# Performance work log

Measured on AMD Instinct MI355X. Metric: run time of the kernel, lower is better.

## Reference

```python
import jax, jax.numpy as jnp
import numpy as np

NH, NP, NL, ED = 8, 8, 1, 256  # num_heads, num_sam_pts, num_levels, embed_dim
EPS = 1e-5


def setup_inputs() -> dict:
    key = jax.random.key(0)
    ks = jax.random.split(key, 6)
    bs, h, w = 8, 64, 64
    d = ED // NH
    return {
        "query": jax.random.normal(ks[0], (bs, 1, ED), jnp.float32),
        "single_feat": jax.random.normal(ks[1], (bs, h * w, NH, d), jnp.float32),
        "ref_2d": jax.random.uniform(ks[2], (bs, h * w, NL, 2), jnp.float32),
        "W_off": jax.random.normal(ks[3], (ED, NH * NL * NP * 2), jnp.float32) * 0.02,
        "b_off": jnp.zeros((NH * NL * NP * 2,), jnp.float32),
        "W_attn": jax.random.normal(ks[4], (ED, NH * NL * NP), jnp.float32) * 0.02,
        "b_attn": jnp.zeros((NH * NL * NP,), jnp.float32),
        "ln_g": jnp.ones((ED,), jnp.float32),
        "ln_b": jnp.zeros((ED,), jnp.float32),
        "h": h,
        "w": w,
    }


def reference(query, single_feat, ref_2d, W_off, b_off, W_attn, b_attn, ln_g, ln_b, h, w):
    bs, nq, _, d = single_feat.shape
    # query: [bs,1,ED] repeated over all h*w query positions
    q = jnp.broadcast_to(query, (bs, h * w, ED))

    # sampling offsets (relu'd, normalized by (w,h)) added to reference points
    off = jax.nn.relu(q @ W_off + b_off).reshape(bs, nq, NH, NL, NP, 2)
    offset_normalizer = jnp.array([w, h], dtype=q.dtype)  # (w, h) order as in torch
    loc = ref_2d[:, :, None, :, None, :] + off / offset_normalizer  # [bs,nq,NH,NL,NP,2]

    # attention weights: relu then softmax over points (last axis)
    aw = jax.nn.relu(q @ W_attn + b_attn).reshape(bs, nq, NH, NL, NP)
    aw = jax.nn.softmax(aw, axis=-1)

    # single-level bilinear grid_sample (align_corners=False, zero padding)
    g = 2.0 * loc[:, :, :, 0] - 1.0  # level 0 -> [bs,nq,NH,NP,2]
    x = (g[..., 0] + 1.0) * (w / 2.0) - 0.5  # pixel coords
    y = (g[..., 1] + 1.0) * (h / 2.0) - 0.5
    x0 = jnp.floor(x)
    y0 = jnp.floor(y)
    x0i = x0.astype(jnp.int32)
    y0i = y0.astype(jnp.int32)

    v = single_feat.transpose(0, 2, 1, 3)  # [bs,NH,H*W,d]

    def gather(xi, yi):
        valid = (xi >= 0) & (xi < w) & (yi >= 0) & (yi < h)  # [bs,nq,NH,NP]
        idx = jnp.clip(yi, 0, h - 1) * w + jnp.clip(xi, 0, w - 1)
        idx = idx.transpose(0, 2, 1, 3).reshape(bs, NH, nq * NP, 1)
        s = jnp.take_along_axis(v, idx, axis=2).reshape(bs, NH, nq, NP, d)
        return s * valid.transpose(0, 2, 1, 3)[..., None].astype(s.dtype)

    wx = (x - x0).transpose(0, 2, 1, 3)[..., None]  # [bs,NH,nq,NP,1]
    wy = (y - y0).transpose(0, 2, 1, 3)[..., None]
    s00 = gather(x0i, y0i)
    s01 = gather(x0i + 1, y0i)
    s10 = gather(x0i, y0i + 1)
    s11 = gather(x0i + 1, y0i + 1)
    top = s00 * (1.0 - wx) + s01 * wx
    bot = s10 * (1.0 - wx) + s11 * wx
    sampled = top * (1.0 - wy) + bot * wy  # [bs,NH,nq,NP,d]

    # weighted sum over points, merge heads
    out = jnp.einsum('bhqpd,bqhp->bqhd', sampled, aw[:, :, :, 0]).reshape(bs, nq, NH * d)

    # norm(dropout(output) + query) -- dropout is identity in eval mode
    res = out + q
    mu = res.mean(-1, keepdims=True)
    var = res.var(-1, keepdims=True)
    return (res - mu) / jnp.sqrt(var + EPS) * ln_g + ln_b
```

## Files before the change

kernel.cpp:

```cpp
#include <hip/hip_runtime.h>

#define ED 256
#define NHEAD 8
#define NPTS 8
#define DHEAD 32

__global__ __launch_bounds__(256) void precompute_kernel(
    const float* __restrict__ query,
    const float* __restrict__ W_off, const float* __restrict__ b_off,
    const float* __restrict__ W_attn, const float* __restrict__ b_attn,
    float* __restrict__ ws)
{
    const int b = blockIdx.x;
    const int t = threadIdx.x;
    __shared__ float sq[ED];
    __shared__ float sattn[NHEAD * NPTS];

    sq[t] = query[b * ED + t];
    __syncthreads();

    if (t < 128) {
        float a0 = 0.f, a1 = 0.f, a2 = 0.f, a3 = 0.f;
        #pragma unroll 4
        for (int k = 0; k < ED; k += 4) {
            a0 = fmaf(sq[k + 0], W_off[(k + 0) * 128 + t], a0);
            a1 = fmaf(sq[k + 1], W_off[(k + 1) * 128 + t], a1);
            a2 = fmaf(sq[k + 2], W_off[(k + 2) * 128 + t], a2);
            a3 = fmaf(sq[k + 3], W_off[(k + 3) * 128 + t], a3);
        }
        ws[b * 192 + t] = fmaxf(b_off[t] + ((a0 + a1) + (a2 + a3)), 0.0f);
    } else if (t < 192) {
        const int j = t - 128;
        float a0 = 0.f, a1 = 0.f, a2 = 0.f, a3 = 0.f;
        #pragma unroll 4
        for (int k = 0; k < ED; k += 4) {
            a0 = fmaf(sq[k + 0], W_attn[(k + 0) * 64 + j], a0);
            a1 = fmaf(sq[k + 1], W_attn[(k + 1) * 64 + j], a1);
            a2 = fmaf(sq[k + 2], W_attn[(k + 2) * 64 + j], a2);
            a3 = fmaf(sq[k + 3], W_attn[(k + 3) * 64 + j], a3);
        }
        sattn[j] = fmaxf(b_attn[j] + ((a0 + a1) + (a2 + a3)), 0.0f);
    }
    __syncthreads();

    if (t >= 128 && t < 192) {
        const int j = t - 128;
        const int hh = j >> 3;
        float m = -1e30f;
        #pragma unroll
        for (int p = 0; p < NPTS; ++p) m = fmaxf(m, sattn[hh * NPTS + p]);
        float s = 0.0f;
        #pragma unroll
        for (int p = 0; p < NPTS; ++p) s += expf(sattn[hh * NPTS + p] - m);
        ws[b * 192 + 128 + j] = expf(sattn[j] - m) / s;
    }
}

__global__ __launch_bounds__(256) void deform_attn_kernel(
    const float* __restrict__ feat,
    const float* __restrict__ ref2d,
    const float* __restrict__ query,
    const float* __restrict__ ln_g, const float* __restrict__ ln_b,
    const float* __restrict__ ws,
    const int* __restrict__ Hp, const int* __restrict__ Wp,
    float* __restrict__ out,
    int nq, int bs)
{
    const int blk = blockIdx.x;
    const int b = blk % bs;
    const int qgroup = blk / bs;
    const int t = threadIdx.x;

    __shared__ float s_off[128];
    __shared__ float s_aw[64];
    __shared__ float s_ref[8];
    __shared__ __align__(16) float s_c[4 * 64 * 8];

    if (t < 128)      s_off[t] = ws[b * 192 + t];
    else if (t < 192) s_aw[t - 128] = ws[b * 192 + t];
    else if (t < 200) {
        const int i = t - 192;
        s_ref[i] = ref2d[(b * nq + qgroup * 4 + (i >> 1)) * 2 + (i & 1)];
    }
    const int H = Hp[0];
    const int W = Wp[0];
    __syncthreads();

    {
        const int qL = t >> 6;
        const int hp = t & 63;
        const int p  = hp & 7;
        const int h  = hp >> 3;

        const float x = s_ref[qL * 2 + 0] * (float)W - 0.5f + s_off[hp * 2 + 0];
        const float y = s_ref[qL * 2 + 1] * (float)H - 0.5f + s_off[hp * 2 + 1];
        const float aw = s_aw[hp];

        const float xf = floorf(x);
        const float yf = floorf(y);
        const int ix = (int)xf;
        const int iy = (int)yf;
        const float wx = x - xf;
        const float wy = y - yf;

        const bool vx0 = (ix >= 0) && (ix < W);
        const bool vx1 = (ix + 1 >= 0) && (ix + 1 < W);
        const bool vy0 = (iy >= 0) && (iy < H);
        const bool vy1 = (iy + 1 >= 0) && (iy + 1 < H);
        const int cx0 = min(max(ix, 0), W - 1);
        const int cx1 = min(max(ix + 1, 0), W - 1);
        const int cy0 = min(max(iy, 0), H - 1);
        const int cy1 = min(max(iy + 1, 0), H - 1);

        const int r0 = cy0 * W;
        const int r1 = cy1 * W;
        int4 idx;
        idx.x = r0 + cx0;
        idx.y = r0 + cx1;
        idx.z = r1 + cx0;
        idx.w = r1 + cx1;

        const float awx = aw * wx, awix = aw - awx;
        float4 wt;
        wt.x = (vx0 && vy0) ? awix * (1.0f - wy) : 0.0f;
        wt.y = (vx1 && vy0) ? awx  * (1.0f - wy) : 0.0f;
        wt.z = (vx0 && vy1) ? awix * wy          : 0.0f;
        wt.w = (vx1 && vy1) ? awx  * wy          : 0.0f;

        const int e = ((qL * 8 + p) * 8 + h) * 8;
        *(int4*)  (&s_c[e])     = idx;
        *(float4*)(&s_c[e + 4]) = wt;
    }
    __syncthreads();

    const int qL   = t >> 6;
    const int lane = t & 63;
    const int h    = lane >> 3;
    const int c4   = lane & 7;
    const int q    = qgroup * 4 + qL;

    const float* fb = feat + (size_t)b * nq * ED + h * DHEAD + c4 * 4;

    float ax = 0.f, ay = 0.f, az = 0.f, aww = 0.f;
    #pragma unroll
    for (int p = 0; p < NPTS; ++p) {
        const int e = ((qL * 8 + p) * 8 + h) * 8;
        const int4   idx = *(const int4*)  (&s_c[e]);
        const float4 wt  = *(const float4*)(&s_c[e + 4]);

        const float4 v0 = *(const float4*)(fb + (size_t)idx.x * ED);
        const float4 v1 = *(const float4*)(fb + (size_t)idx.y * ED);
        const float4 v2 = *(const float4*)(fb + (size_t)idx.z * ED);
        const float4 v3 = *(const float4*)(fb + (size_t)idx.w * ED);

        ax = fmaf(wt.x, v0.x, ax); ay = fmaf(wt.x, v0.y, ay);
        az = fmaf(wt.x, v0.z, az); aww = fmaf(wt.x, v0.w, aww);
        ax = fmaf(wt.y, v1.x, ax); ay = fmaf(wt.y, v1.y, ay);
        az = fmaf(wt.y, v1.z, az); aww = fmaf(wt.y, v1.w, aww);
        ax = fmaf(wt.z, v2.x, ax); ay = fmaf(wt.z, v2.y, ay);
        az = fmaf(wt.z, v2.z, az); aww = fmaf(wt.z, v2.w, aww);
        ax = fmaf(wt.w, v3.x, ax); ay = fmaf(wt.w, v3.y, ay);
        az = fmaf(wt.w, v3.z, az); aww = fmaf(wt.w, v3.w, aww);
    }

    const float4 qv = *(const float4*)(query + b * ED + lane * 4);
    const float r0 = ax + qv.x;
    const float r1 = ay + qv.y;
    const float r2 = az + qv.z;
    const float r3 = aww + qv.w;

    float s  = (r0 + r1) + (r2 + r3);
    float ss = fmaf(r0, r0, fmaf(r1, r1, fmaf(r2, r2, r3 * r3)));
    #pragma unroll
    for (int m = 1; m < 64; m <<= 1) {
        s  += __shfl_xor(s, m, 64);
        ss += __shfl_xor(ss, m, 64);
    }
    const float mean = s * (1.0f / ED);
    const float var  = ss * (1.0f / ED) - mean * mean;
    const float inv  = rsqrtf(var + 1e-5f);

    const float4 g = *(const float4*)(ln_g + lane * 4);
    const float4 be = *(const float4*)(ln_b + lane * 4);
    float4 o;
    o.x = (r0 - mean) * inv * g.x + be.x;
    o.y = (r1 - mean) * inv * g.y + be.y;
    o.z = (r2 - mean) * inv * g.z + be.z;
    o.w = (r3 - mean) * inv * g.w + be.w;
    *(float4*)(out + ((size_t)b * nq + q) * ED + lane * 4) = o;
}

extern "C" void kernel_launch(void* const* d_in, const int* in_sizes, int n_in,
                              void* d_out, int out_size, void* d_ws, size_t ws_size,
                              hipStream_t stream)
{
    const float* query  = (const float*)d_in[0];
    const float* feat   = (const float*)d_in[1];
    const float* ref2d  = (const float*)d_in[2];
    const float* W_off  = (const float*)d_in[3];
    const float* b_off  = (const float*)d_in[4];
    const float* W_attn = (const float*)d_in[5];
    const float* b_attn = (const float*)d_in[6];
    const float* ln_g   = (const float*)d_in[7];
    const float* ln_b   = (const float*)d_in[8];
    const int*   Hp     = (const int*)d_in[9];
    const int*   Wp     = (const int*)d_in[10];
    float* out = (float*)d_out;
    float* ws  = (float*)d_ws;

    const int bs = in_sizes[0] / ED;
    const int nq = in_sizes[2] / (bs * 2);

    precompute_kernel<<<bs, 256, 0, stream>>>(query, W_off, b_off, W_attn, b_attn, ws);
    deform_attn_kernel<<<bs * nq / 4, 256, 0, stream>>>(feat, ref2d, query, ln_g, ln_b,
                                                        ws, Hp, Wp, out, nq, bs);
}
```

Before: 145.5 us.

## Process eight queries per block and software-pipeline feature gathers across points

Each block now handles eight query positions instead of four, looping twice over groups of four per thread and hoisting the query, gamma and beta loads out of the loop. Inside the point loop, the gathers for the next sampling point are issued before the FMAs on the current one, so load latency overlaps with arithmetic. The aim is to amortise per-block setup and improve memory-level parallelism. The cost is more registers, a larger shared buffer and half as many blocks, which may reduce occupancy and parallelism.

```diff
diff --git a/kernel.cpp b/kernel.cpp
--- a/kernel.cpp
+++ b/kernel.cpp
@@ -4,6 +4,7 @@
 #define NHEAD 8
 #define NPTS 8
 #define DHEAD 32
+#define QPB 8
 
 __global__ __launch_bounds__(256) void precompute_kernel(
     const float* __restrict__ query,
@@ -68,27 +69,28 @@
 {
     const int blk = blockIdx.x;
     const int b = blk % bs;
-    const int qgroup = blk / bs;
+    const int qbase = (blk / bs) * QPB;
     const int t = threadIdx.x;
 
     __shared__ float s_off[128];
     __shared__ float s_aw[64];
-    __shared__ float s_ref[8];
-    __shared__ __align__(16) float s_c[4 * 64 * 8];
+    __shared__ float s_ref[QPB * 2];
+    __shared__ __align__(16) float s_c[QPB * 64 * 8];
 
     if (t < 128)      s_off[t] = ws[b * 192 + t];
     else if (t < 192) s_aw[t - 128] = ws[b * 192 + t];
-    else if (t < 200) {
+    else if (t < 192 + QPB * 2) {
         const int i = t - 192;
-        s_ref[i] = ref2d[(b * nq + qgroup * 4 + (i >> 1)) * 2 + (i & 1)];
+        s_ref[i] = ref2d[(b * nq + qbase + (i >> 1)) * 2 + (i & 1)];
     }
     const int H = Hp[0];
     const int W = Wp[0];
     __syncthreads();
 
-    {
-        const int qL = t >> 6;
-        const int hp = t & 63;
+    #pragma unroll
+    for (int u = t; u < QPB * 64; u += 256) {
+        const int qL = u >> 6;
+        const int hp = u & 63;
         const int p  = hp & 7;
         const int h  = hp >> 3;
 
@@ -127,7 +129,7 @@
         wt.z = (vx0 && vy1) ? awix * wy          : 0.0f;
         wt.w = (vx1 && vy1) ? awx  * wy          : 0.0f;
 
-        const int e = ((qL * 8 + p) * 8 + h) * 8;
+        const int e = (qL * 64 + p * 8 + h) * 8;
         *(int4*)  (&s_c[e])     = idx;
         *(float4*)(&s_c[e + 4]) = wt;
     }
@@ -137,57 +139,77 @@
     const int lane = t & 63;
     const int h    = lane >> 3;
     const int c4   = lane & 7;
-    const int q    = qgroup * 4 + qL;
 
     const float* fb = feat + (size_t)b * nq * ED + h * DHEAD + c4 * 4;
-
-    float ax = 0.f, ay = 0.f, az = 0.f, aww = 0.f;
+    const float4 qv = *(const float4*)(query + b * ED + lane * 4);
+    const float4 g  = *(const float4*)(ln_g + lane * 4);
+    const float4 be = *(const float4*)(ln_b + lane * 4);
+
     #pragma unroll
-    for (int p = 0; p < NPTS; ++p) {
-        const int e = ((qL * 8 + p) * 8 + h) * 8;
-        const int4   idx = *(const int4*)  (&s_c[e]);
-        const float4 wt  = *(const float4*)(&s_c[e + 4]);
-
-        const float4 v0 = *(const float4*)(fb + (size_t)idx.x * ED);
-        const float4 v1 = *(const float4*)(fb + (size_t)idx.y * ED);
-        const float4 v2 = *(const float4*)(fb + (size_t)idx.z * ED);
-        const float4 v3 = *(const float4*)(fb + (size_t)idx.w * ED);
-
-        ax = fmaf(wt.x, v0.x, ax); ay = fmaf(wt.x, v0.y, ay);
-        az = fmaf(wt.x, v0.z, az); aww = fmaf(wt.x, v0.w, aww);
-        ax = fmaf(wt.y, v1.x, ax); ay = fmaf(wt.y, v1.y, ay);
-        az = fmaf(wt.y, v1.z, az); aww = fmaf(wt.y, v1.w, aww);
-        ax = fmaf(wt.z, v2.x, ax); ay = fmaf(wt.z, v2.y, ay);
-        az = fmaf(wt.z, v2.z, az); aww = fmaf(wt.z, v2.w, aww);
-        ax = fmaf(wt.w, v3.x, ax); ay = fmaf(wt.w, v3.y, ay);
-        az = fmaf(wt.w, v3.z, az); aww = fmaf(wt.w, v3.w, aww);
-    }
-
-    const float4 qv = *(const float4*)(query + b * ED + lane * 4);
-    const float r0 = ax + qv.x;
-    const float r1 = ay + qv.y;
-    const float r2 = az + qv.z;
-    const float r3 = aww + qv.w;
-
-    float s  = (r0 + r1) + (r2 + r3);
-    float ss = fmaf(r0, r0, fmaf(r1, r1, fmaf(r2, r2, r3 * r3)));
-    #pragma unroll
-    for (int m = 1; m < 64; m <<= 1) {
-        s  += __shfl_xor(s, m, 64);
-        ss += __shfl_xor(ss, m, 64);
-    }
-    const float mean = s * (1.0f / ED);
-    const float var  = ss * (1.0f / ED) - mean * mean;
-    const float inv  = rsqrtf(var + 1e-5f);
-
-    const float4 g = *(const float4*)(ln_g + lane * 4);
-    const float4 be = *(const float4*)(ln_b + lane * 4);
-    float4 o;
-    o.x = (r0 - mean) * inv * g.x + be.x;
-    o.y = (r1 - mean) * inv * g.y + be.y;
-    o.z = (r2 - mean) * inv * g.z + be.z;
-    o.w = (r3 - mean) * inv * g.w + be.w;
-    *(float4*)(out + ((size_t)b * nq + q) * ED + lane * 4) = o;
+    for (int gq = 0; gq < QPB / 4; ++gq) {
+        const int qloc = gq * 4 + qL;
+        const int q = qbase + qloc;
+        const int cb = qloc * 512;
+
+        float ax = 0.f, ay = 0.f, az = 0.f, aw4 = 0.f;
+
+        int4   idxA = *(const int4*)  (&s_c[cb + h * 8]);
+        float4 wtA  = *(const float4*)(&s_c[cb + h * 8 + 4]);
+        float4 v0 = *(const float4*)(fb + (size_t)idxA.x * ED);
+        float4 v1 = *(const float4*)(fb + (size_t)idxA.y * ED);
+        float4 v2 = *(const float4*)(fb + (size_t)idxA.z * ED);
+        float4 v3 = *(const float4*)(fb + (size_t)idxA.w * ED);
+
+        #pragma unroll
+        for (int p = 0; p < NPTS; ++p) {
+            int4 idxB; float4 wtB;
+            float4 u0, u1, u2, u3;
+            if (p < NPTS - 1) {
+                const int e = cb + (p + 1) * 64 + h * 8;
+                idxB = *(const int4*)  (&s_c[e]);
+                wtB  = *(const float4*)(&s_c[e + 4]);
+                u0 = *(const float4*)(fb + (size_t)idxB.x * ED);
+                u1 = *(const float4*)(fb + (size_t)idxB.y * ED);
+                u2 = *(const float4*)(fb + (size_t)idxB.z * ED);
+                u3 = *(const float4*)(fb + (size_t)idxB.w * ED);
+            }
+            ax = fmaf(wtA.x, v0.x, ax); ay = fmaf(wtA.x, v0.y, ay);
+            az = fmaf(wtA.x, v0.z, az); aw4 = fmaf(wtA.x, v0.w, aw4);
+            ax = fmaf(wtA.y, v1.x, ax); ay = fmaf(wtA.y, v1.y, ay);
+            az = fmaf(wtA.y, v1.z, az); aw4 = fmaf(wtA.y, v1.w, aw4);
+            ax = fmaf(wtA.z, v2.x, ax); ay = fmaf(wtA.z, v2.y, ay);
+            az = fmaf(wtA.z, v2.z, az); aw4 = fmaf(wtA.z, v2.w, aw4);
+            ax = fmaf(wtA.w, v3.x, ax); ay = fmaf(wtA.w, v3.y, ay);
+            az = fmaf(wtA.w, v3.z, az); aw4 = fmaf(wtA.w, v3.w, aw4);
+            if (p < NPTS - 1) {
+                idxA = idxB; wtA = wtB;
+                v0 = u0; v1 = u1; v2 = u2; v3 = u3;
+            }
+        }
+
+        const float r0 = ax + qv.x;
+        const float r1 = ay + qv.y;
+        const float r2 = az + qv.z;
+        const float r3 = aw4 + qv.w;
+
+        float s  = (r0 + r1) + (r2 + r3);
+        float ss = fmaf(r0, r0, fmaf(r1, r1, fmaf(r2, r2, r3 * r3)));
+        #pragma unroll
+        for (int m = 1; m < 64; m <<= 1) {
+            s  += __shfl_xor(s, m, 64);
+            ss += __shfl_xor(ss, m, 64);
+        }
+        const float mean = s * (1.0f / ED);
+        const float var  = ss * (1.0f / ED) - mean * mean;
+        const float inv  = rsqrtf(var + 1e-5f);
+
+        float4 o;
+        o.x = (r0 - mean) * inv * g.x + be.x;
+        o.y = (r1 - mean) * inv * g.y + be.y;
+        o.z = (r2 - mean) * inv * g.z + be.z;
+        o.w = (r3 - mean) * inv * g.w + be.w;
+        *(float4*)(out + ((size_t)b * nq + q) * ED + lane * 4) = o;
+    }
 }
 
 extern "C" void kernel_launch(void* const* d_in, const int* in_sizes, int n_in,
@@ -212,6 +234,6 @@
     const int nq = in_sizes[2] / (bs * 2);
 
     precompute_kernel<<<bs, 256, 0, stream>>>(query, W_off, b_off, W_attn, b_attn, ws);
-    deform_attn_kernel<<<bs * nq / 4, 256, 0, stream>>>(feat, ref2d, query, ln_g, ln_b,
-                                                        ws, Hp, Wp, out, nq, bs);
+    deform_attn_kernel<<<bs * nq / QPB, 256, 0, stream>>>(feat, ref2d, query, ln_g, ln_b,
+                                                          ws, Hp, Wp, out, nq, bs);
 }
```

Result: no change. 146.6 us (+0.8%).
